# Optimization experiments

Hardware: AMD Instinct MI355X
Metric: run time of the kernel (lower is better)

The kernel has to match this reference:

```python
import jax, jax.numpy as jnp
import numpy as np

EPS = 1e-3  # kernel epsilon used in Performer generalized kernel
B, H, N, D, M = 1, 8, 1024, 64, 128  # batch, heads, seq, dim_heads, nb_features


def _gaussian_orthogonal_matrix(m, d, seed=0):
    # GaussianOrthogonalRandomMatrix with scaling=0: stacked QR blocks, rows
    # rescaled by chi-distributed norms of gaussian d-vectors.
    rng = np.random.default_rng(seed)
    blocks = []
    for _ in range(m // d):
        g = rng.standard_normal((d, d))
        qmat, _ = np.linalg.qr(g)
        blocks.append(qmat.T)
    proj = np.concatenate(blocks, axis=0)  # [m, d], orthonormal rows per block
    mult = np.linalg.norm(rng.standard_normal((m, d)), axis=1)  # chi norms
    return (mult[:, None] * proj).astype(np.float32)


def setup_inputs() -> dict:
    key = jax.random.key(0)
    kq, kk, kv = jax.random.split(key, 3)
    q = jax.random.normal(kq, (B, H, N, D), dtype=jnp.float32)
    k = jax.random.normal(kk, (B, H, N, D), dtype=jnp.float32)
    v = jax.random.normal(kv, (B, H, N, D), dtype=jnp.float32)
    proj = jnp.asarray(_gaussian_orthogonal_matrix(M, D))
    return {"q": q, "k": k, "v": v, "proj": proj}


def _generalized_kernel(x, proj):
    # kernel_fn(relu)( (x / d**0.25) @ proj^T ) + eps
    normalizer = 1.0 / (x.shape[-1] ** 0.25)
    xp = jnp.einsum('bhnd,md->bhnm', x * normalizer, proj)
    return jax.nn.relu(xp) + EPS


def reference(q, k, v, proj):
    qp = _generalized_kernel(q, proj)  # [B,H,N,M]
    kp = _generalized_kernel(k, proj)  # [B,H,N,M]
    # causal linear attention
    k_cumsum = jnp.cumsum(kp, axis=-2)                              # [B,H,N,M]
    context = jnp.einsum('bhnm,bhne->bhnme', kp, v)                 # [B,H,N,M,D]
    context = jnp.cumsum(context, axis=-3)                          # prefix sums over n
    context = context / k_cumsum[..., None]                         # normalize
    out = jnp.einsum('bhnme,bhnm->bhne', context, qp)               # [B,H,N,D]
    return out
```

## Files before the change

### kernel.cpp

```cpp
#include <hip/hip_runtime.h>

static constexpr int H = 8, N = 1024, D = 64, M = 128, CHUNK = 128, NC = 8;
static constexpr float EPS = 1e-3f;
static constexpr float NORM = 0.35355339059327373f;

typedef __attribute__((ext_vector_type(8))) short short8;
typedef __attribute__((ext_vector_type(4))) float f32x4;

__device__ inline unsigned short f2bf(float x) {
    unsigned u = __float_as_uint(x);
    return (unsigned short)((u + 0x7fffu + ((u >> 16) & 1u)) >> 16);
}
__device__ inline float bf2f(unsigned short u) {
    return __uint_as_float(((unsigned)u) << 16);
}
__device__ inline ushort4 pack4(float4 g) {
    return (ushort4){f2bf(g.x), f2bf(g.y), f2bf(g.z), f2bf(g.w)};
}

__global__ __launch_bounds__(256) void k_projg(const float* __restrict__ q,
                                               const float* __restrict__ k,
                                               const float* __restrict__ proj,
                                               const float* __restrict__ v,
                                               unsigned short* __restrict__ qpb,
                                               unsigned short* __restrict__ kpb,
                                               unsigned short* __restrict__ Gpb,
                                               float* __restrict__ kpart) {
    __shared__ __align__(16) short smem[19200];
    short* projb = smem;
    short* xb = smem + 9216;
    short* kpT = smem + 11520;
    short* vT = smem + 16640;
    const int tid = threadIdx.x;
    const int rblk = blockIdx.x;
    const int h = blockIdx.y;
    const int which = blockIdx.z;
    const float* __restrict__ x = which ? k : q;
    unsigned short* __restrict__ dst = which ? kpb : qpb;
    const int rowbase = h * N + rblk * 32;
    const int lane = tid & 63, wv = tid >> 6;
    const int rt = wv & 1, mh = wv >> 1;
    const int fr = lane & 15, fq = lane >> 4;

    for (int i4 = tid; i4 < 2048; i4 += 256) {
        int m = i4 >> 4, dq = i4 & 15;
        float4 g = *(const float4*)&proj[i4 * 4];
        *(ushort4*)&projb[m * 72 + dq * 4] = pack4(g);
    }
    for (int i4 = tid; i4 < 512; i4 += 256) {
        int r = i4 >> 4, dq = i4 & 15;
        float4 g = *(const float4*)&x[(rowbase + r) * D + dq * 4];
        g.x *= NORM; g.y *= NORM; g.z *= NORM; g.w *= NORM;
        *(ushort4*)&xb[r * 72 + dq * 4] = pack4(g);
    }
    if (which) {
        for (int i4 = tid; i4 < 512; i4 += 256) {
            int r = i4 & 31, e4 = (i4 >> 5) * 4;
            float4 g = *(const float4*)&v[(rowbase + r) * D + e4];
            vT[(e4 + 0) * 40 + r] = (short)f2bf(g.x);
            vT[(e4 + 1) * 40 + r] = (short)f2bf(g.y);
            vT[(e4 + 2) * 40 + r] = (short)f2bf(g.z);
            vT[(e4 + 3) * 40 + r] = (short)f2bf(g.w);
        }
    }
    __syncthreads();

    f32x4 accp[4];
#pragma unroll
    for (int i = 0; i < 4; i++) accp[i] = (f32x4){0.f, 0.f, 0.f, 0.f};
#pragma unroll
    for (int kt = 0; kt < 2; kt++) {
        short8 a = *(const short8*)&xb[(16 * rt + fr) * 72 + kt * 32 + fq * 8];
#pragma unroll
        for (int i = 0; i < 4; i++) {
            const int mt = mh * 4 + i;
            short8 bb = *(const short8*)&projb[(16 * mt + fr) * 72 + kt * 32 + fq * 8];
            accp[i] = __builtin_amdgcn_mfma_f32_16x16x32_bf16(a, bb, accp[i], 0, 0, 0);
        }
    }
#pragma unroll
    for (int i = 0; i < 4; i++) {
        const int mt = mh * 4 + i;
#pragma unroll
        for (int reg = 0; reg < 4; reg++) {
            const int r = 16 * rt + fq * 4 + reg;
            const int m = 16 * mt + fr;
            unsigned short bv = f2bf(fmaxf(accp[i][reg], 0.f) + EPS);
            dst[(rowbase + r) * M + m] = bv;
            if (which) kpT[m * 40 + r] = (short)bv;
        }
    }
    if (!which) return;
    __syncthreads();

    const int gb = h * 32 + rblk;
    f32x4 gacc[2][4];
#pragma unroll
    for (int i = 0; i < 2; i++)
#pragma unroll
        for (int et = 0; et < 4; et++) gacc[i][et] = (f32x4){0.f, 0.f, 0.f, 0.f};
#pragma unroll
    for (int i = 0; i < 2; i++) {
        const int mt = wv * 2 + i;
        short8 a = *(const short8*)&kpT[(16 * mt + fr) * 40 + fq * 8];
#pragma unroll
        for (int et = 0; et < 4; et++) {
            short8 bb = *(const short8*)&vT[(16 * et + fr) * 40 + fq * 8];
            gacc[i][et] =
                __builtin_amdgcn_mfma_f32_16x16x32_bf16(a, bb, gacc[i][et], 0, 0, 0);
        }
    }
#pragma unroll
    for (int i = 0; i < 2; i++) {
        const int mt = wv * 2 + i;
#pragma unroll
        for (int et = 0; et < 4; et++)
#pragma unroll
            for (int reg = 0; reg < 4; reg++) {
                const int m = 16 * mt + fq * 4 + reg;
                const int e = 16 * et + fr;
                Gpb[(gb * M + m) * D + e] = f2bf(gacc[i][et][reg]);
            }
    }
    if (tid < 128) {
        float ks = 0.f;
#pragma unroll 8
        for (int r = 0; r < 32; r++) ks += bf2f(kpT[tid * 40 + r]);
        kpart[gb * M + tid] = ks;
    }
}

__global__ __launch_bounds__(512) void k_attn(const unsigned short* __restrict__ qpb,
                                              const unsigned short* __restrict__ kpb,
                                              const float* __restrict__ kpart,
                                              const unsigned short* __restrict__ Gpb,
                                              const float* __restrict__ v,
                                              float* __restrict__ out) {
    __shared__ __align__(16) short smem[26112];
    short* bufA = smem;
    short* bufB = smem + 4352;
    short* bufC = smem + 21760;
    const int tid = threadIdx.x;
    const int b = blockIdx.x;
    const int sub = blockIdx.y;
    const int h = b >> 3, c = 7 - (b & 7);
    const int chunkbase = h * N + c * CHUNK;
    const int rowstart = chunkbase + sub * 32;
    const int lane = tid & 63, wv = tid >> 6;
    const int rt = wv & 1, js = wv >> 1;
    const int fr = lane & 15, fq = lane >> 4;

    {
        const unsigned int* src = (const unsigned int*)kpb;
        for (int i = tid; i < 8192; i += 512) {
            int j = i >> 6, mu = i & 63;
            ((unsigned int*)&bufB[j * 136])[mu] = src[(chunkbase + j) * 64 + mu];
        }
    }
    if (tid < 128) {
        const int m = tid;
        float z = 0.f;
        const int send = c * 4 + sub;
        for (int s = 0; s < send; s++) z += kpart[(h * 32 + s) * M + m];
        unsigned short kr_[32], qr_[32];
#pragma unroll
        for (int r = 0; r < 32; r++) {
            kr_[r] = kpb[(rowstart + r) * M + m];
            qr_[r] = qpb[(rowstart + r) * M + m];
        }
#pragma unroll
        for (int r = 0; r < 32; r++) {
            z += bf2f(kr_[r]);
            bufA[r * 136 + m] =
                (short)f2bf(bf2f(qr_[r]) * __builtin_amdgcn_rcpf(z));
        }
    }
    float s0r[16];
#pragma unroll
    for (int j = 0; j < 16; j++) s0r[j] = 0.f;
    for (int cp = 0; cp < c; cp++) {
#pragma unroll
        for (int p = 0; p < 4; p++) {
            const short* gsrc =
                (const short*)&Gpb[(h * 32 + cp * 4 + p) * (M * D) + tid * 16];
            short8 g0 = *(const short8*)&gsrc[0];
            short8 g1 = *(const short8*)&gsrc[8];
#pragma unroll
            for (int j = 0; j < 8; j++) {
                s0r[j] += bf2f((unsigned short)g0[j]);
                s0r[8 + j] += bf2f((unsigned short)g1[j]);
            }
        }
    }
    __syncthreads();

    const int jtmax = 2 * sub + 2;
    f32x4 acc1[2];
    acc1[0] = (f32x4){0.f, 0.f, 0.f, 0.f};
    acc1[1] = (f32x4){0.f, 0.f, 0.f, 0.f};
#pragma unroll
    for (int kt = 0; kt < 4; kt++) {
        short8 a = *(const short8*)&bufA[(16 * rt + fr) * 136 + kt * 32 + fq * 8];
#pragma unroll
        for (int jl = 0; jl < 2; jl++) {
            const int jt = 2 * js + jl;
            if (jt < jtmax) {
                short8 bb =
                    *(const short8*)&bufB[(16 * jt + fr) * 136 + kt * 32 + fq * 8];
                acc1[jl] =
                    __builtin_amdgcn_mfma_f32_16x16x32_bf16(a, bb, acc1[jl], 0, 0, 0);
            }
        }
    }
#pragma unroll
    for (int jl = 0; jl < 2; jl++) {
        const int jt = 2 * js + jl;
        if (jt < jtmax) {
            const int j = 16 * jt + fr;
#pragma unroll
            for (int reg = 0; reg < 4; reg++) {
                const int nloc = 16 * rt + fq * 4 + reg;
                float val = (j <= sub * 32 + nloc) ? acc1[jl][reg] : 0.f;
                bufC[nloc * 136 + j] = (short)f2bf(val);
            }
        }
    }
    __syncthreads();

    {
        const int m = tid >> 2;
        const int ebase = (tid & 3) * 16;
#pragma unroll
        for (int j = 0; j < 16; j++)
            bufB[(ebase + j) * 136 + m] = (short)f2bf(s0r[j]);
    }
    __syncthreads();

    f32x4 acc2 = (f32x4){0.f, 0.f, 0.f, 0.f};
#pragma unroll
    for (int kt = 0; kt < 4; kt++) {
        short8 a = *(const short8*)&bufA[(16 * rt + fr) * 136 + kt * 32 + fq * 8];
        short8 bb = *(const short8*)&bufB[(16 * js + fr) * 136 + kt * 32 + fq * 8];
        acc2 = __builtin_amdgcn_mfma_f32_16x16x32_bf16(a, bb, acc2, 0, 0, 0);
    }
    __syncthreads();

    for (int i = tid; i < 2048; i += 512) {
        int j = i >> 4, e4 = (i & 15) * 4;
        float4 g = *(const float4*)&v[(chunkbase + j) * D + e4];
        bufB[(e4 + 0) * 136 + j] = (short)f2bf(g.x);
        bufB[(e4 + 1) * 136 + j] = (short)f2bf(g.y);
        bufB[(e4 + 2) * 136 + j] = (short)f2bf(g.z);
        bufB[(e4 + 3) * 136 + j] = (short)f2bf(g.w);
    }
    __syncthreads();

    const int ktmax = sub + 1;
    for (int kt = 0; kt < ktmax; kt++) {
        short8 a = *(const short8*)&bufC[(16 * rt + fr) * 136 + kt * 32 + fq * 8];
        short8 bb = *(const short8*)&bufB[(16 * js + fr) * 136 + kt * 32 + fq * 8];
        acc2 = __builtin_amdgcn_mfma_f32_16x16x32_bf16(a, bb, acc2, 0, 0, 0);
    }

#pragma unroll
    for (int reg = 0; reg < 4; reg++) {
        out[(rowstart + 16 * rt + fq * 4 + reg) * D + 16 * js + fr] = acc2[reg];
    }
}

extern "C" void kernel_launch(void* const* d_in, const int* in_sizes, int n_in,
                              void* d_out, int out_size, void* d_ws, size_t ws_size,
                              hipStream_t stream) {
    const float* q = (const float*)d_in[0];
    const float* k = (const float*)d_in[1];
    const float* v = (const float*)d_in[2];
    const float* proj = (const float*)d_in[3];
    float* out = (float*)d_out;

    float* ws = (float*)d_ws;
    float* kpart = ws;
    unsigned short* qpb = (unsigned short*)(kpart + H * 32 * M);
    unsigned short* kpb = qpb + H * N * M;
    unsigned short* Gpb = kpb + H * N * M;

    k_projg<<<dim3(32, H, 2), 256, 0, stream>>>(q, k, proj, v, qpb, kpb, Gpb,
                                                kpart);
    k_attn<<<dim3(H * NC, 4), 512, 0, stream>>>(qpb, kpb, kpart, Gpb, v, out);
}
```

Before: 89.73 us.

## Merge q/k projection blocks and stage outputs through LDS for coalesced stores

```diff
diff --git a/kernel.cpp b/kernel.cpp
--- a/kernel.cpp
+++ b/kernel.cpp
@@ -18,7 +18,7 @@
     return (ushort4){f2bf(g.x), f2bf(g.y), f2bf(g.z), f2bf(g.w)};
 }
 
-__global__ __launch_bounds__(256) void k_projg(const float* __restrict__ q,
+__global__ __launch_bounds__(512) void k_projg(const float* __restrict__ q,
                                                const float* __restrict__ k,
                                                const float* __restrict__ proj,
                                                const float* __restrict__ v,
@@ -26,42 +26,38 @@
                                                unsigned short* __restrict__ kpb,
                                                unsigned short* __restrict__ Gpb,
                                                float* __restrict__ kpart) {
-    __shared__ __align__(16) short smem[19200];
+    __shared__ __align__(16) short smem[30208];
     short* projb = smem;
     short* xb = smem + 9216;
-    short* kpT = smem + 11520;
-    short* vT = smem + 16640;
+    short* obuf = smem + 13824;
+    short* kpT = smem + 22528;
+    short* vT = smem + 27648;
     const int tid = threadIdx.x;
     const int rblk = blockIdx.x;
     const int h = blockIdx.y;
-    const int which = blockIdx.z;
-    const float* __restrict__ x = which ? k : q;
-    unsigned short* __restrict__ dst = which ? kpb : qpb;
     const int rowbase = h * N + rblk * 32;
     const int lane = tid & 63, wv = tid >> 6;
-    const int rt = wv & 1, mh = wv >> 1;
+    const int rt = wv & 3, mh = wv >> 2;
     const int fr = lane & 15, fq = lane >> 4;
 
-    for (int i4 = tid; i4 < 2048; i4 += 256) {
+    for (int i4 = tid; i4 < 2048; i4 += 512) {
         int m = i4 >> 4, dq = i4 & 15;
-        float4 g = *(const float4*)&proj[i4 * 4];
-        *(ushort4*)&projb[m * 72 + dq * 4] = pack4(g);
-    }
-    for (int i4 = tid; i4 < 512; i4 += 256) {
-        int r = i4 >> 4, dq = i4 & 15;
-        float4 g = *(const float4*)&x[(rowbase + r) * D + dq * 4];
+        *(ushort4*)&projb[m * 72 + dq * 4] = pack4(*(const float4*)&proj[i4 * 4]);
+    }
+    {
+        int r = tid >> 4, dq = tid & 15;
+        float4 g = *(const float4*)&q[(rowbase + r) * D + dq * 4];
         g.x *= NORM; g.y *= NORM; g.z *= NORM; g.w *= NORM;
         *(ushort4*)&xb[r * 72 + dq * 4] = pack4(g);
-    }
-    if (which) {
-        for (int i4 = tid; i4 < 512; i4 += 256) {
-            int r = i4 & 31, e4 = (i4 >> 5) * 4;
-            float4 g = *(const float4*)&v[(rowbase + r) * D + e4];
-            vT[(e4 + 0) * 40 + r] = (short)f2bf(g.x);
-            vT[(e4 + 1) * 40 + r] = (short)f2bf(g.y);
-            vT[(e4 + 2) * 40 + r] = (short)f2bf(g.z);
-            vT[(e4 + 3) * 40 + r] = (short)f2bf(g.w);
-        }
+        float4 gk = *(const float4*)&k[(rowbase + r) * D + dq * 4];
+        gk.x *= NORM; gk.y *= NORM; gk.z *= NORM; gk.w *= NORM;
+        *(ushort4*)&xb[(32 + r) * 72 + dq * 4] = pack4(gk);
+        int rv = tid & 31, e4 = (tid >> 5) * 4;
+        float4 gv = *(const float4*)&v[(rowbase + rv) * D + e4];
+        vT[(e4 + 0) * 40 + rv] = (short)f2bf(gv.x);
+        vT[(e4 + 1) * 40 + rv] = (short)f2bf(gv.y);
+        vT[(e4 + 2) * 40 + rv] = (short)f2bf(gv.z);
+        vT[(e4 + 3) * 40 + rv] = (short)f2bf(gv.w);
     }
     __syncthreads();
 
@@ -86,47 +82,50 @@
             const int r = 16 * rt + fq * 4 + reg;
             const int m = 16 * mt + fr;
             unsigned short bv = f2bf(fmaxf(accp[i][reg], 0.f) + EPS);
-            dst[(rowbase + r) * M + m] = bv;
-            if (which) kpT[m * 40 + r] = (short)bv;
-        }
-    }
-    if (!which) return;
-    __syncthreads();
-
+            obuf[r * 136 + m] = (short)bv;
+            if (rt >= 2) kpT[m * 40 + (r - 32)] = (short)bv;
+        }
+    }
+    __syncthreads();
+
+    for (int i = tid; i < 2048; i += 512) {
+        int r = i >> 5, cu = i & 31;
+        ushort4 val = *(const ushort4*)&obuf[r * 136 + cu * 4];
+        unsigned short* g = (r < 32) ? &qpb[(rowbase + r) * M + cu * 4]
+                                     : &kpb[(rowbase + r - 32) * M + cu * 4];
+        *(ushort4*)g = val;
+    }
     const int gb = h * 32 + rblk;
-    f32x4 gacc[2][4];
-#pragma unroll
-    for (int i = 0; i < 2; i++)
-#pragma unroll
-        for (int et = 0; et < 4; et++) gacc[i][et] = (f32x4){0.f, 0.f, 0.f, 0.f};
-#pragma unroll
-    for (int i = 0; i < 2; i++) {
-        const int mt = wv * 2 + i;
-        short8 a = *(const short8*)&kpT[(16 * mt + fr) * 40 + fq * 8];
-#pragma unroll
-        for (int et = 0; et < 4; et++) {
-            short8 bb = *(const short8*)&vT[(16 * et + fr) * 40 + fq * 8];
-            gacc[i][et] =
-                __builtin_amdgcn_mfma_f32_16x16x32_bf16(a, bb, gacc[i][et], 0, 0, 0);
-        }
-    }
-#pragma unroll
-    for (int i = 0; i < 2; i++) {
-        const int mt = wv * 2 + i;
-#pragma unroll
-        for (int et = 0; et < 4; et++)
-#pragma unroll
-            for (int reg = 0; reg < 4; reg++) {
-                const int m = 16 * mt + fq * 4 + reg;
-                const int e = 16 * et + fr;
-                Gpb[(gb * M + m) * D + e] = f2bf(gacc[i][et][reg]);
-            }
-    }
     if (tid < 128) {
         float ks = 0.f;
 #pragma unroll 8
-        for (int r = 0; r < 32; r++) ks += bf2f(kpT[tid * 40 + r]);
+        for (int r = 0; r < 32; r++) ks += bf2f((unsigned short)kpT[tid * 40 + r]);
         kpart[gb * M + tid] = ks;
+    }
+    __syncthreads();
+
+    f32x4 gacc[4];
+#pragma unroll
+    for (int et = 0; et < 4; et++) gacc[et] = (f32x4){0.f, 0.f, 0.f, 0.f};
+    {
+        short8 a = *(const short8*)&kpT[(16 * wv + fr) * 40 + fq * 8];
+#pragma unroll
+        for (int et = 0; et < 4; et++) {
+            short8 bb = *(const short8*)&vT[(16 * et + fr) * 40 + fq * 8];
+            gacc[et] = __builtin_amdgcn_mfma_f32_16x16x32_bf16(a, bb, gacc[et], 0, 0, 0);
+        }
+    }
+#pragma unroll
+    for (int et = 0; et < 4; et++)
+#pragma unroll
+        for (int reg = 0; reg < 4; reg++) {
+            const int m = 16 * wv + fq * 4 + reg;
+            obuf[m * 68 + 16 * et + fr] = (short)f2bf(gacc[et][reg]);
+        }
+    __syncthreads();
+    for (int i = tid; i < 2048; i += 512) {
+        int m = i >> 4, e4 = (i & 15) * 4;
+        *(ushort4*)&Gpb[(gb * M + m) * D + e4] = *(const ushort4*)&obuf[m * 68 + e4];
     }
 }
 
@@ -156,23 +155,24 @@
             int j = i >> 6, mu = i & 63;
             ((unsigned int*)&bufB[j * 136])[mu] = src[(chunkbase + j) * 64 + mu];
         }
-    }
+        const unsigned int* srcq = (const unsigned int*)qpb;
+        for (int i = tid; i < 2048; i += 512) {
+            int r = i >> 6, mu = i & 63;
+            ((unsigned int*)&bufC[r * 136])[mu] = srcq[(rowstart + r) * 64 + mu];
+        }
+    }
+    __syncthreads();
+
     if (tid < 128) {
         const int m = tid;
         float z = 0.f;
         const int send = c * 4 + sub;
         for (int s = 0; s < send; s++) z += kpart[(h * 32 + s) * M + m];
-        unsigned short kr_[32], qr_[32];
-#pragma unroll
+#pragma unroll 8
         for (int r = 0; r < 32; r++) {
-            kr_[r] = kpb[(rowstart + r) * M + m];
-            qr_[r] = qpb[(rowstart + r) * M + m];
-        }
-#pragma unroll
-        for (int r = 0; r < 32; r++) {
-            z += bf2f(kr_[r]);
-            bufA[r * 136 + m] =
-                (short)f2bf(bf2f(qr_[r]) * __builtin_amdgcn_rcpf(z));
+            z += bf2f((unsigned short)bufB[(sub * 32 + r) * 136 + m]);
+            bufA[r * 136 + m] = (short)f2bf(
+                bf2f((unsigned short)bufC[r * 136 + m]) * __builtin_amdgcn_rcpf(z));
         }
     }
     float s0r[16];
@@ -212,6 +212,7 @@
             }
         }
     }
+    __syncthreads();
 #pragma unroll
     for (int jl = 0; jl < 2; jl++) {
         const int jt = 2 * js + jl;
@@ -225,7 +226,6 @@
             }
         }
     }
-    __syncthreads();
 
     {
         const int m = tid >> 2;
@@ -283,7 +283,7 @@
     unsigned short* kpb = qpb + H * N * M;
     unsigned short* Gpb = kpb + H * N * M;
 
-    k_projg<<<dim3(32, H, 2), 256, 0, stream>>>(q, k, proj, v, qpb, kpb, Gpb,
-                                                kpart);
+    k_projg<<<dim3(32, H), 512, 0, stream>>>(q, k, proj, v, qpb, kpb, Gpb,
+                                             kpart);
     k_attn<<<dim3(H * NC, 4), 512, 0, stream>>>(qpb, kpb, kpart, Gpb, v, out);
 }
```

Result: no change. 89.80 us (+0.1%).
